# Kernel tuning notes

Measured on AMD Instinct MI355X. Metric: run time of the kernel, lower is better.

Reference implementation:

```python
import jax, jax.numpy as jnp
import numpy as np

B, T, C = 4, 2048, 1024
H, DK, DV = 16, 64, 64  # num_heads, qk_length, value_length (must be equal per source bug)


def setup_inputs() -> dict:
    key = jax.random.key(0)
    ks = jax.random.split(key, 11)
    s = 0.02
    return {
        "Q": jax.random.normal(ks[0], (B, T, C), jnp.float32),
        "K": jax.random.normal(ks[1], (B, T, C), jnp.float32),
        "V": jax.random.normal(ks[2], (B, T, C), jnp.float32),
        "Wq": jax.random.normal(ks[3], (C, H * DK), jnp.float32) * s,
        "bq": jnp.zeros((H * DK,), jnp.float32),
        "Wk": jax.random.normal(ks[4], (C, H * DK), jnp.float32) * s,
        "bk": jnp.zeros((H * DK,), jnp.float32),
        "Wv": jax.random.normal(ks[5], (C, H * DK), jnp.float32) * s,
        "bv": jnp.zeros((H * DK,), jnp.float32),
        "Wo": jax.random.normal(ks[6], (H * DV, C), jnp.float32) * s,
        "bo": jnp.zeros((C,), jnp.float32),
    }


def _split_heads(x, d):
    # (B, T, H*d) -> (B, H, T, d)
    b, t, _ = x.shape
    return x.reshape(b, t, H, d).transpose(0, 2, 1, 3)


def reference(Q, K, V, Wq, bq, Wk, bk, Wv, bv, Wo, bo):
    q = _split_heads(Q @ Wq + bq, DK)  # (B,H,T,DK)
    k = _split_heads(K @ Wk + bk, DK)
    v = _split_heads(V @ Wv + bv, DV)
    scores = jnp.einsum("bhqd,bhkd->bhqk", q, k) / jnp.sqrt(jnp.float32(DK))
    weights = jax.nn.softmax(scores, axis=-1)  # materialized (B,H,T,T) as in source
    attn = jnp.einsum("bhqk,bhkd->bhqd", weights, v)  # (B,H,T,DV)
    # Faithful to source combine_heads: raw view (B,H,T,DV) -> (B,T,H*DV) WITHOUT transposing
    out = attn.reshape(B, T, H * DV)
    return out @ Wo + bo
```

## Files before the change

### kernel.cpp

```cpp
#include <hip/hip_runtime.h>

typedef unsigned short u16;
typedef __attribute__((ext_vector_type(8))) short bf16x8;
typedef __attribute__((ext_vector_type(4))) float f32x4;

__device__ __forceinline__ u16 f2bf(float f) {
  union { float fv; unsigned u; } v; v.fv = f;
  unsigned r = v.u + 0x7fffu + ((v.u >> 16) & 1u);
  return (u16)(r >> 16);
}

__device__ __forceinline__ unsigned pkbf(float a, float b) {
  union { float f; unsigned u; } ua, ub;
  ua.f = a; ub.f = b;
  return ((ub.u + 0x8000u) & 0xFFFF0000u) | ((ua.u + 0x8000u) >> 16);
}

__device__ __forceinline__ void gload_lds16(const void* g, void* l) {
  __builtin_amdgcn_global_load_lds(
      (const __attribute__((address_space(1))) unsigned*)g,
      (__attribute__((address_space(3))) unsigned*)l, 16, 0, 0);
}

__device__ __forceinline__ int swz128(int o) { return o ^ ((o >> 3) & 0x70); }

__global__ __launch_bounds__(256) void transpose_cvt4_kernel(
    const float* __restrict__ W0, const float* __restrict__ W1,
    const float* __restrict__ W2, const float* __restrict__ W3,
    u16* __restrict__ T0, u16* __restrict__ T1,
    u16* __restrict__ T2, u16* __restrict__ T3) {
  __shared__ float tile[32][33];
  const int z = blockIdx.z;
  const float* W = z == 0 ? W0 : z == 1 ? W1 : z == 2 ? W2 : W3;
  u16* WT = z == 0 ? T0 : z == 1 ? T1 : z == 2 ? T2 : T3;
  const int bx = blockIdx.x * 32, by = blockIdx.y * 32;
  const int tx = threadIdx.x, ty = threadIdx.y;
  #pragma unroll
  for (int i = 0; i < 32; i += 8)
    tile[ty + i][tx] = W[(size_t)(by + ty + i) * 1024 + bx + tx];
  __syncthreads();
  #pragma unroll
  for (int i = 0; i < 32; i += 8)
    WT[(size_t)(bx + ty + i) * 1024 + by + tx] = f2bf(tile[tx][ty + i]);
}

__global__ __launch_bounds__(256) void proj_gemm_kernel(
    const float* __restrict__ Qf, const float* __restrict__ Kf,
    const float* __restrict__ Vf,
    const u16* __restrict__ WTq, const u16* __restrict__ WTk,
    const u16* __restrict__ WTv,
    const float* __restrict__ bqp, const float* __restrict__ bkp,
    const float* __restrict__ bvp,
    u16* __restrict__ qhd, u16* __restrict__ khd, u16* __restrict__ vtd) {
  __shared__ u16 As[128 * 32];
  __shared__ u16 Bs[128 * 32];
  const int tid = threadIdx.x;
  const int w = tid >> 6, lane = tid & 63;
  const int wr = w >> 1, wc = w & 1;
  const int l16 = lane & 15, lhi = lane >> 4;
  const int lg = (blockIdx.x & 7) * 192 + (blockIdx.x >> 3);
  const int proj = lg >> 9, inner = lg & 511;
  const int m0 = (inner >> 3) * 128, n0 = (inner & 7) * 128;
  const float* A  = proj == 0 ? Qf : proj == 1 ? Kf : Vf;
  const u16*   BT = proj == 0 ? WTq : proj == 1 ? WTk : WTv;
  const float* bias = proj == 0 ? bqp : proj == 1 ? bkp : bvp;

  const int arow = tid >> 2, ac = (tid & 3) * 8;

  f32x4 acc[4][4] = {};

  for (int kt = 0; kt < 32; ++kt) {
    #pragma unroll
    for (int i = 0; i < 2; ++i) {
      const int ob = w * 2048 + i * 1024;
      const int o = ob + (lane << 4);
      const int row = o >> 6, kbyte = o & 63;
      gload_lds16((const char*)BT + (((size_t)(n0 + row)) << 11) + (kt << 6) + kbyte,
                  (char*)Bs + ob);
    }
    #pragma unroll
    for (int i = 0; i < 2; ++i) {
      const int r = arow + i * 64;
      const float* ap = A + (size_t)(m0 + r) * 1024 + kt * 32 + ac;
      const float4 v0 = *(const float4*)(ap);
      const float4 v1 = *(const float4*)(ap + 4);
      uint4 pk;
      pk.x = pkbf(v0.x, v0.y); pk.y = pkbf(v0.z, v0.w);
      pk.z = pkbf(v1.x, v1.y); pk.w = pkbf(v1.z, v1.w);
      *(uint4*)((char*)As + r * 64 + ac * 2) = pk;
    }
    __syncthreads();
    bf16x8 a[4], b[4];
    #pragma unroll
    for (int i = 0; i < 4; ++i)
      a[i] = *(const bf16x8*)(As + (wr * 64 + i * 16 + l16) * 32 + lhi * 8);
    #pragma unroll
    for (int j = 0; j < 4; ++j)
      b[j] = *(const bf16x8*)(Bs + (wc * 64 + j * 16 + l16) * 32 + lhi * 8);
    #pragma unroll
    for (int i = 0; i < 4; ++i)
      #pragma unroll
      for (int j = 0; j < 4; ++j)
        acc[i][j] = __builtin_amdgcn_mfma_f32_16x16x32_bf16(a[i], b[j], acc[i][j], 0, 0, 0);
    __syncthreads();
  }

  #pragma unroll
  for (int i = 0; i < 4; ++i) {
    #pragma unroll
    for (int j = 0; j < 4; ++j) {
      const int n = (inner & 7) * 128 + wc * 64 + j * 16 + l16;
      const float bn = bias[n];
      #pragma unroll
      for (int r = 0; r < 4; ++r) {
        const int m = m0 + wr * 64 + i * 16 + lhi * 4 + r;
        float v = acc[i][j][r] + bn;
        const int bb = m >> 11, t = m & 2047, h = n >> 6, d = n & 63;
        if (proj == 0) {
          v *= 0.18033688f;
          qhd[((((size_t)bb * 16 + h) * 2048 + t) << 6) + d] = f2bf(v);
        } else if (proj == 1) {
          khd[((((size_t)bb * 16 + h) * 2048 + t) << 6) + d] = f2bf(v);
        } else {
          vtd[(((size_t)bb * 16 + h) * 64 + d) * 2048 + t] = f2bf(v);
        }
      }
    }
  }
}

__global__ __launch_bounds__(256) void out_gemm_kernel(
    const u16* __restrict__ A, const u16* __restrict__ BT,
    const float* __restrict__ bias, float* __restrict__ out) {
  __shared__ u16 As[128 * 32];
  __shared__ u16 Bs[128 * 32];
  const int tid = threadIdx.x;
  const int w = tid >> 6, lane = tid & 63;
  const int wr = w >> 1, wc = w & 1;
  const int l16 = lane & 15, lhi = lane >> 4;
  const int lg = (blockIdx.x & 7) * 64 + (blockIdx.x >> 3);
  const int m0 = (lg >> 3) * 128, n0 = (lg & 7) * 128;

  f32x4 acc[4][4] = {};

  for (int kt = 0; kt < 32; ++kt) {
    #pragma unroll
    for (int i = 0; i < 2; ++i) {
      const int ob = w * 2048 + i * 1024;
      const int o = ob + (lane << 4);
      const int row = o >> 6, kbyte = o & 63;
      gload_lds16((const char*)A + (((size_t)(m0 + row)) << 11) + (kt << 6) + kbyte,
                  (char*)As + ob);
      gload_lds16((const char*)BT + (((size_t)(n0 + row)) << 11) + (kt << 6) + kbyte,
                  (char*)Bs + ob);
    }
    __syncthreads();
    bf16x8 a[4], b[4];
    #pragma unroll
    for (int i = 0; i < 4; ++i)
      a[i] = *(const bf16x8*)(As + (wr * 64 + i * 16 + l16) * 32 + lhi * 8);
    #pragma unroll
    for (int j = 0; j < 4; ++j)
      b[j] = *(const bf16x8*)(Bs + (wc * 64 + j * 16 + l16) * 32 + lhi * 8);
    #pragma unroll
    for (int i = 0; i < 4; ++i)
      #pragma unroll
      for (int j = 0; j < 4; ++j)
        acc[i][j] = __builtin_amdgcn_mfma_f32_16x16x32_bf16(a[i], b[j], acc[i][j], 0, 0, 0);
    __syncthreads();
  }

  #pragma unroll
  for (int i = 0; i < 4; ++i) {
    #pragma unroll
    for (int j = 0; j < 4; ++j) {
      const int n = n0 + wc * 64 + j * 16 + l16;
      const float bn = bias[n];
      #pragma unroll
      for (int r = 0; r < 4; ++r) {
        const int m = m0 + wr * 64 + i * 16 + lhi * 4 + r;
        out[(size_t)m * 1024 + n] = acc[i][j][r] + bn;
      }
    }
  }
}

__global__ __launch_bounds__(512) void attn_kernel(
    const u16* __restrict__ qh, const u16* __restrict__ kh,
    const u16* __restrict__ vth, u16* __restrict__ outPre) {
  __shared__ u16 Kbuf[2][64 * 64];
  __shared__ u16 Vbuf[64 * 64];
  __shared__ u16 Pl[8][16 * 64];

  const int tid = threadIdx.x, w = tid >> 6, lane = tid & 63;
  const int l16 = lane & 15, lhi = lane >> 4;

  const int wg = (blockIdx.x & 7) * 128 + (blockIdx.x >> 3);
  const int qt = wg & 15, hb = wg >> 4;
  const int h = hb & 15, b = hb >> 4;

  const size_t bh = (size_t)b * 16 + h;
  const u16* qb = qh + bh * (2048 * 64);
  const u16* kb = kh + bh * (2048 * 64);
  const u16* vb = vth + bh * (64 * 2048);

  const int qr0 = qt * 128 + w * 16;
  bf16x8 aq[2];
  #pragma unroll
  for (int c = 0; c < 2; ++c)
    aq[c] = *(const bf16x8*)(qb + (qr0 + l16) * 64 + c * 32 + lhi * 8);

  bf16x8 ones;
  #pragma unroll
  for (int e = 0; e < 8; ++e) ones[e] = (short)0x3F80;

  f32x4 acc_o[4] = {};
  f32x4 acc_l = {};

  auto stageK = [&](int buf, int kv) {
    char* Kt = (char*)&Kbuf[buf][0];
    const int ob = w * 1024;
    const int os = swz128(ob + (lane << 4));
    gload_lds16((const char*)kb + ((size_t)kv << 7) + os, Kt + ob);
  };
  auto stageV = [&](int kv) {
    char* Vt = (char*)&Vbuf[0];
    const int ob = w * 1024;
    const int os = swz128(ob + (lane << 4));
    const int dd = os >> 7, j0 = (os & 127) >> 1;
    gload_lds16((const char*)vb + ((size_t)dd << 12) + (((size_t)(kv + j0)) << 1),
                Vt + ob);
  };

  stageK(0, 0);

  for (int t = 0; t < 32; ++t) {
    const int buf = t & 1;
    __syncthreads();
    stageV(t * 64);

    const char* Kt = (const char*)&Kbuf[buf][0];

    f32x4 s[4];
    #pragma unroll
    for (int jt = 0; jt < 4; ++jt) s[jt] = f32x4{-4.f, -4.f, -4.f, -4.f};
    __builtin_amdgcn_s_setprio(1);
    #pragma unroll
    for (int c = 0; c < 2; ++c) {
      #pragma unroll
      for (int jt = 0; jt < 4; ++jt) {
        const bf16x8 bk = *(const bf16x8*)(Kt +
            swz128((jt * 16 + l16) * 128 + c * 64 + lhi * 16));
        s[jt] = __builtin_amdgcn_mfma_f32_16x16x32_bf16(aq[c], bk, s[jt], 0, 0, 0);
      }
    }
    __builtin_amdgcn_s_setprio(0);

    #pragma unroll
    for (int jt = 0; jt < 4; ++jt)
      #pragma unroll
      for (int r = 0; r < 4; ++r)
        s[jt][r] = __builtin_amdgcn_exp2f(s[jt][r]);

    char* Pw = (char*)&Pl[w][0];
    #pragma unroll
    for (int jt = 0; jt < 4; ++jt)
      #pragma unroll
      for (int r = 0; r < 4; ++r) {
        union { float f; unsigned u; } pv;
        pv.f = s[jt][r];
        *(u16*)(Pw + swz128((lhi * 4 + r) * 128 + (jt * 16 + l16) * 2)) =
            (u16)((pv.u + 0x8000u) >> 16);
      }

    __syncthreads();
    if (t < 31) stageK(buf ^ 1, (t + 1) * 64);

    const char* Vt = (const char*)&Vbuf[0];

    __builtin_amdgcn_s_setprio(1);
    #pragma unroll
    for (int c = 0; c < 2; ++c) {
      const bf16x8 ap = *(const bf16x8*)(Pw +
          swz128(l16 * 128 + c * 64 + lhi * 16));
      acc_l = __builtin_amdgcn_mfma_f32_16x16x32_bf16(ap, ones, acc_l, 0, 0, 0);
      #pragma unroll
      for (int dt = 0; dt < 4; ++dt) {
        const bf16x8 bv = *(const bf16x8*)(Vt +
            swz128((dt * 16 + l16) * 128 + c * 64 + lhi * 16));
        acc_o[dt] = __builtin_amdgcn_mfma_f32_16x16x32_bf16(ap, bv, acc_o[dt], 0, 0, 0);
      }
    }
    __builtin_amdgcn_s_setprio(0);
  }

  #pragma unroll
  for (int dt = 0; dt < 4; ++dt) {
    #pragma unroll
    for (int r = 0; r < 4; ++r) {
      const int t = qr0 + lhi * 4 + r;
      const int d = dt * 16 + l16;
      const float v = acc_o[dt][r] / acc_l[r];
      const int rr = h * 128 + (t >> 4);
      const int cc = ((t & 15) << 6) + d;
      outPre[((size_t)b * 2048 + rr) * 1024 + cc] = f2bf(v);
    }
  }
}

extern "C" void kernel_launch(void* const* d_in, const int* in_sizes, int n_in,
                              void* d_out, int out_size, void* d_ws, size_t ws_size,
                              hipStream_t stream) {
  const float* Q  = (const float*)d_in[0];
  const float* K  = (const float*)d_in[1];
  const float* V  = (const float*)d_in[2];
  const float* Wq = (const float*)d_in[3];
  const float* bq = (const float*)d_in[4];
  const float* Wk = (const float*)d_in[5];
  const float* bk = (const float*)d_in[6];
  const float* Wv = (const float*)d_in[7];
  const float* bv = (const float*)d_in[8];
  const float* Wo = (const float*)d_in[9];
  const float* bo = (const float*)d_in[10];

  char* ws = (char*)d_ws;
  const size_t ACT = 16777216;
  u16* act = (u16*)(ws);
  u16* qhd = (u16*)(ws + ACT);
  u16* khd = (u16*)(ws + 2 * ACT);
  u16* vtd = (u16*)(ws + 3 * ACT);
  u16* wtq = (u16*)(ws);
  u16* wtk = (u16*)(ws + 2097152);
  u16* wtv = (u16*)(ws + 2 * 2097152);
  u16* wto = (u16*)(ws + 4 * ACT);

  transpose_cvt4_kernel<<<dim3(32, 32, 4), dim3(32, 8), 0, stream>>>(
      Wq, Wk, Wv, Wo, wtq, wtk, wtv, wto);
  proj_gemm_kernel<<<1536, 256, 0, stream>>>(Q, K, V, wtq, wtk, wtv,
                                             bq, bk, bv, qhd, khd, vtd);
  attn_kernel<<<1024, 512, 0, stream>>>(qhd, khd, vtd, act);
  out_gemm_kernel<<<512, 256, 0, stream>>>(act, wto, bo, (float*)d_out);
}
```

Measured before the change: 240.3 us.

## Swizzle GEMM LDS tiles and prefetch fp32 A tiles into registers

Adds an XOR swizzle for the 64-byte-row LDS tiles in the QKV and output projection GEMMs. It is applied both to the global-to-LDS direct loads (by permuting source addresses) and to the MFMA fragment reads, to cut LDS bank conflicts. The QKV GEMM also register-prefetches the next k-tile of fp32 activations after the barrier, so global latency overlaps with MFMA work. This costs extra registers and adds swizzle address arithmetic.

Result: no change. 241.5 us, median of 2 (+0.5%).

```diff
diff --git a/kernel.cpp b/kernel.cpp
--- a/kernel.cpp
+++ b/kernel.cpp
@@ -23,6 +23,7 @@
 }
 
 __device__ __forceinline__ int swz128(int o) { return o ^ ((o >> 3) & 0x70); }
+__device__ __forceinline__ int swz64(int o) { return o ^ (((o >> 7) & 3) << 4); }
 
 __global__ __launch_bounds__(256) void transpose_cvt4_kernel(
     const float* __restrict__ W0, const float* __restrict__ W1,
@@ -68,35 +69,48 @@
   const int arow = tid >> 2, ac = (tid & 3) * 8;
 
   f32x4 acc[4][4] = {};
+  float4 pre[2][2];
+
+  auto loadA = [&](int kt) {
+    #pragma unroll
+    for (int i = 0; i < 2; ++i) {
+      const float* ap = A + (size_t)(m0 + arow + i * 64) * 1024 + kt * 32 + ac;
+      pre[i][0] = *(const float4*)(ap);
+      pre[i][1] = *(const float4*)(ap + 4);
+    }
+  };
+
+  loadA(0);
 
   for (int kt = 0; kt < 32; ++kt) {
+    #pragma unroll
+    for (int i = 0; i < 2; ++i) {
+      uint4 pk;
+      pk.x = pkbf(pre[i][0].x, pre[i][0].y); pk.y = pkbf(pre[i][0].z, pre[i][0].w);
+      pk.z = pkbf(pre[i][1].x, pre[i][1].y); pk.w = pkbf(pre[i][1].z, pre[i][1].w);
+      const int lb = (arow + i * 64) * 64 + (tid & 3) * 16;
+      *(uint4*)((char*)As + swz64(lb)) = pk;
+    }
     #pragma unroll
     for (int i = 0; i < 2; ++i) {
       const int ob = w * 2048 + i * 1024;
-      const int o = ob + (lane << 4);
-      const int row = o >> 6, kbyte = o & 63;
-      gload_lds16((const char*)BT + (((size_t)(n0 + row)) << 11) + (kt << 6) + kbyte,
+      const int os = swz64(ob + (lane << 4));
+      const int row = os >> 6, kb = os & 63;
+      gload_lds16((const char*)BT + (((size_t)(n0 + row)) << 11) + (kt << 6) + kb,
                   (char*)Bs + ob);
     }
-    #pragma unroll
-    for (int i = 0; i < 2; ++i) {
-      const int r = arow + i * 64;
-      const float* ap = A + (size_t)(m0 + r) * 1024 + kt * 32 + ac;
-      const float4 v0 = *(const float4*)(ap);
-      const float4 v1 = *(const float4*)(ap + 4);
-      uint4 pk;
-      pk.x = pkbf(v0.x, v0.y); pk.y = pkbf(v0.z, v0.w);
-      pk.z = pkbf(v1.x, v1.y); pk.w = pkbf(v1.z, v1.w);
-      *(uint4*)((char*)As + r * 64 + ac * 2) = pk;
-    }
-    __syncthreads();
+    __syncthreads();
+    if (kt < 31) loadA(kt + 1);
+
     bf16x8 a[4], b[4];
     #pragma unroll
     for (int i = 0; i < 4; ++i)
-      a[i] = *(const bf16x8*)(As + (wr * 64 + i * 16 + l16) * 32 + lhi * 8);
+      a[i] = *(const bf16x8*)((const char*)As +
+             swz64((wr * 64 + i * 16 + l16) * 64 + lhi * 16));
     #pragma unroll
     for (int j = 0; j < 4; ++j)
-      b[j] = *(const bf16x8*)(Bs + (wc * 64 + j * 16 + l16) * 32 + lhi * 8);
+      b[j] = *(const bf16x8*)((const char*)Bs +
+             swz64((wc * 64 + j * 16 + l16) * 64 + lhi * 16));
     #pragma unroll
     for (int i = 0; i < 4; ++i)
       #pragma unroll
@@ -109,7 +123,7 @@
   for (int i = 0; i < 4; ++i) {
     #pragma unroll
     for (int j = 0; j < 4; ++j) {
-      const int n = (inner & 7) * 128 + wc * 64 + j * 16 + l16;
+      const int n = n0 + wc * 64 + j * 16 + l16;
       const float bn = bias[n];
       #pragma unroll
       for (int r = 0; r < 4; ++r) {
@@ -147,21 +161,23 @@
     #pragma unroll
     for (int i = 0; i < 2; ++i) {
       const int ob = w * 2048 + i * 1024;
-      const int o = ob + (lane << 4);
-      const int row = o >> 6, kbyte = o & 63;
-      gload_lds16((const char*)A + (((size_t)(m0 + row)) << 11) + (kt << 6) + kbyte,
+      const int os = swz64(ob + (lane << 4));
+      const int row = os >> 6, kb = os & 63;
+      gload_lds16((const char*)A + (((size_t)(m0 + row)) << 11) + (kt << 6) + kb,
                   (char*)As + ob);
-      gload_lds16((const char*)BT + (((size_t)(n0 + row)) << 11) + (kt << 6) + kbyte,
+      gload_lds16((const char*)BT + (((size_t)(n0 + row)) << 11) + (kt << 6) + kb,
                   (char*)Bs + ob);
     }
     __syncthreads();
     bf16x8 a[4], b[4];
     #pragma unroll
     for (int i = 0; i < 4; ++i)
-      a[i] = *(const bf16x8*)(As + (wr * 64 + i * 16 + l16) * 32 + lhi * 8);
+      a[i] = *(const bf16x8*)((const char*)As +
+             swz64((wr * 64 + i * 16 + l16) * 64 + lhi * 16));
     #pragma unroll
     for (int j = 0; j < 4; ++j)
-      b[j] = *(const bf16x8*)(Bs + (wc * 64 + j * 16 + l16) * 32 + lhi * 8);
+      b[j] = *(const bf16x8*)((const char*)Bs +
+             swz64((wc * 64 + j * 16 + l16) * 64 + lhi * 16));
     #pragma unroll
     for (int i = 0; i < 4; ++i)
       #pragma unroll
```
